# Performance work log

Hardware: AMD Instinct MI355X
Metric: run time of the kernel (lower is better)

## Reference

```python
import math
import jax, jax.numpy as jnp
import numpy as np
from jax import lax

B = 8
IN_CH = 512
OUT_CH = 256
K = 3
LATENT = 512
BLUR = [1, 3, 3, 1]
FACTOR = 2
H = W = 64
# p = len(blur) - factor - (K-1) = 0 -> pad = ((p+1)//2 + factor - 1, p//2 + 1) = (1, 1)
PAD0, PAD1 = 1, 1


def _make_blur_kernel():
    k = jnp.array(BLUR, jnp.float32)
    k = k[None, :] * k[:, None]          # separable -> 2D
    k = k / jnp.sum(k)
    return k * (FACTOR ** 2)             # make_kernel(blur, factor) scales by factor^2


def setup_inputs() -> dict:
    key = jax.random.key(0)
    k1, k2, k3, k4 = jax.random.split(key, 4)
    inputs = {
        "input": jax.random.normal(k1, (B, IN_CH, H, W), jnp.float32),
        "w": jax.random.normal(k2, (B, LATENT), jnp.float32),
        # learned params
        "affine_weight": jax.random.normal(k3, (IN_CH, LATENT), jnp.float32),
        "affine_bias": jnp.ones((IN_CH,), jnp.float32),  # bias_init=1
        "conv_weight": jax.random.normal(k4, (1, OUT_CH, IN_CH, K, K), jnp.float32),
    }
    return inputs


def reference(input, w, affine_weight, affine_bias, conv_weight):
    batch = input.shape[0]
    # EqualLinear: scale = 1/sqrt(latent_dim), lr_mul=1
    style = w @ (affine_weight * (1.0 / math.sqrt(LATENT))).T + affine_bias  # (B, IN_CH)
    # modulate
    scale = 1.0 / math.sqrt(IN_CH * K * K)
    weight = (scale * conv_weight) * style[:, None, :, None, None]          # (B, OUT, IN, K, K)
    # demodulate over (in, kh, kw)
    demod = lax.rsqrt(jnp.sum(weight * weight, axis=(2, 3, 4)) + 1e-8)      # (B, OUT)
    weight = weight * demod[:, :, None, None, None]
    # grouped conv_transpose2d (groups=batch, stride=2, pad=0) == per-sample
    # conv with lhs_dilation=2, spatial padding K-1, kernel spatially flipped.
    kflip = jnp.flip(weight, (-2, -1))                                      # (B, OUT, IN, K, K) OIHW

    def ct(x, kern):  # x: (IN, H, W), kern: (OUT, IN, K, K)
        return lax.conv_general_dilated(
            x[None], kern, window_strides=(1, 1),
            padding=[(K - 1, K - 1), (K - 1, K - 1)],
            lhs_dilation=(2, 2),
            dimension_numbers=("NCHW", "OIHW", "NCHW"))[0]

    out = jax.vmap(ct)(input, kflip)                                        # (B, OUT, 2H-2+K, 2W-2+K)
    # upfirdn2d with up=down=1: pad then depthwise correlate with flipped FIR kernel
    blur = jnp.flip(_make_blur_kernel())                                    # (4, 4)
    out = jnp.pad(out, ((0, 0), (0, 0), (PAD0, PAD1), (PAD0, PAD1)))
    dw = jnp.tile(blur[None, None], (OUT_CH, 1, 1, 1))                      # (OUT, 1, 4, 4)
    out = lax.conv_general_dilated(
        out, dw, window_strides=(1, 1), padding="VALID",
        feature_group_count=OUT_CH,
        dimension_numbers=("NCHW", "OIHW", "NCHW"))
    return out  # (B, OUT, 2H, 2W)
```

## Files before the change

### kernel.cpp

```cpp
#include <hip/hip_runtime.h>
#include <hip/hip_bf16.h>
#include <math.h>

#define NB 8
#define INCH 512
#define OUTCH 256
#define SP 4096
#define LAT 512
#define NTAP 9
#define MDIM (NTAP*OUTCH)

#define INV_SQRT_LAT 0.044194173824159216f
#define WSCALE 0.014731391274719738f

typedef __bf16 bf16x8 __attribute__((ext_vector_type(8)));
typedef float  f32x4  __attribute__((ext_vector_type(4)));

__device__ __forceinline__ unsigned short f2bf(float f) {
  unsigned u = __float_as_uint(f);
  u += 0x7fffu + ((u >> 16) & 1u);
  return (unsigned short)(u >> 16);
}
__device__ __forceinline__ float bf2f(unsigned short v) {
  return __uint_as_float((unsigned)v << 16);
}

__global__ void prep_k(const float* __restrict__ w, const float* __restrict__ aff,
                       const float* __restrict__ bias, float* __restrict__ style,
                       const float* __restrict__ cw, float* __restrict__ S,
                       unsigned short* __restrict__ w9) {
  if (blockIdx.x < 16) {
    int gid = blockIdx.x * 256 + threadIdx.x;
    int b = gid >> 9, i = gid & 511;
    const float4* wv = (const float4*)(w + (size_t)b * LAT);
    const float4* av = (const float4*)(aff + (size_t)i * LAT);
    float s = 0.f;
#pragma unroll 4
    for (int l = 0; l < LAT / 4; ++l) {
      float4 a = av[l], ww = wv[l];
      s += a.x * ww.x + a.y * ww.y + a.z * ww.z + a.w * ww.w;
    }
    style[gid] = s * INV_SQRT_LAT + bias[i];
  } else {
    int gid = (blockIdx.x - 16) * 256 + threadIdx.x;
    int o = gid >> 9, i = gid & 511;
    const float* p = cw + (size_t)gid * 9;
    float ss = 0.f, v[9];
#pragma unroll
    for (int t = 0; t < 9; ++t) { v[t] = p[t]; ss += v[t] * v[t]; }
    S[gid] = ss * (WSCALE * WSCALE);
#pragma unroll
    for (int t = 0; t < 9; ++t)
      w9[((size_t)(t * OUTCH + o)) * INCH + i] = f2bf(v[t] * WSCALE);
  }
}

__global__ void demod_k(const float* __restrict__ style, const float* __restrict__ S,
                        float* __restrict__ dmod) {
  int gid = blockIdx.x * 256 + threadIdx.x;
  int b = gid >> 8, o = gid & 255;
  const float4* sv = (const float4*)(style + (size_t)b * INCH);
  const float4* Sv = (const float4*)(S + (size_t)o * INCH);
  float acc = 0.f;
#pragma unroll 4
  for (int l = 0; l < INCH / 4; ++l) {
    float4 st = sv[l], s2 = Sv[l];
    acc += st.x * st.x * s2.x + st.y * st.y * s2.y + st.z * st.z * s2.z + st.w * st.w * s2.w;
  }
  dmod[gid] = 1.0f / sqrtf(acc + 1e-8f);
}

__global__ void modx_k(const float* __restrict__ x, const float* __restrict__ style,
                       unsigned short* __restrict__ xmt) {
  __shared__ float tile[32][33];
  int b = blockIdx.z;
  int s0 = blockIdx.x * 32;
  int i0 = blockIdx.y * 32;
  int c = threadIdx.x & 31, r = threadIdx.x >> 5;
#pragma unroll
  for (int p = 0; p < 4; ++p) {
    int ii = r + p * 8;
    tile[ii][c] = x[((size_t)(b * INCH + i0 + ii)) * SP + s0 + c] * style[b * INCH + i0 + ii];
  }
  __syncthreads();
#pragma unroll
  for (int p = 0; p < 4; ++p) {
    int ss = r + p * 8;
    xmt[((size_t)(b * SP + s0 + ss)) * INCH + i0 + c] = f2bf(tile[c][ss]);
  }
}

__global__ __launch_bounds__(256, 2)
void gemm_k(const unsigned short* __restrict__ A,
            const unsigned short* __restrict__ Bm,
            unsigned short* __restrict__ C) {
  __shared__ __align__(16) unsigned short As[128 * 64];
  __shared__ __align__(16) unsigned short Bs[128 * 64];
  __shared__ __align__(16) unsigned short stage[64 * 136];
  Bm += (size_t)blockIdx.z * SP * INCH;
  C  += (size_t)blockIdx.z * MDIM * SP;
  const int tid  = threadIdx.x;
  const int lane = tid & 63;
  const int wave = tid >> 6;
  const int m0 = blockIdx.y * 128;
  const int n0 = blockIdx.x * 128;
  const int wm = (wave >> 1) * 64;
  const int wn = (wave & 1) * 64;
  const int lrow   = lane >> 3;
  const int gchunk = (lane & 7) ^ lrow;

  f32x4 acc[4][4];
#pragma unroll
  for (int i = 0; i < 4; ++i)
#pragma unroll
    for (int j = 0; j < 4; ++j) acc[i][j] = (f32x4){0.f, 0.f, 0.f, 0.f};

  const int r16  = lane & 15;
  const int quad = lane >> 4;

  for (int k0 = 0; k0 < INCH; k0 += 64) {
#pragma unroll
    for (int it = 0; it < 4; ++it) {
      int rbase = it * 32 + wave * 8;
      const unsigned short* ga = A  + (size_t)(m0 + rbase + lrow) * INCH + k0 + gchunk * 8;
      const unsigned short* gb = Bm + (size_t)(n0 + rbase + lrow) * INCH + k0 + gchunk * 8;
      __builtin_amdgcn_global_load_lds((const __attribute__((address_space(1))) void*)ga,
                                       (__attribute__((address_space(3))) void*)&As[rbase * 64],
                                       16, 0, 0);
      __builtin_amdgcn_global_load_lds((const __attribute__((address_space(1))) void*)gb,
                                       (__attribute__((address_space(3))) void*)&Bs[rbase * 64],
                                       16, 0, 0);
    }
    __syncthreads();
#pragma unroll
    for (int kk = 0; kk < 2; ++kk) {
      bf16x8 af[4], bfr[4];
#pragma unroll
      for (int i = 0; i < 4; ++i) {
        int rowa = wm + i * 16 + r16;
        int cha  = (kk * 4 + quad) ^ (rowa & 7);
        af[i] = *(const bf16x8*)&As[rowa * 64 + cha * 8];
        int rowb = wn + i * 16 + r16;
        int chb  = (kk * 4 + quad) ^ (rowb & 7);
        bfr[i] = *(const bf16x8*)&Bs[rowb * 64 + chb * 8];
      }
#pragma unroll
      for (int i = 0; i < 4; ++i)
#pragma unroll
        for (int j = 0; j < 4; ++j)
          acc[i][j] = __builtin_amdgcn_mfma_f32_16x16x32_bf16(af[i], bfr[j], acc[i][j], 0, 0, 0);
    }
    __syncthreads();
  }
#pragma unroll
  for (int p = 0; p < 2; ++p) {
    if ((wave >> 1) == p) {
#pragma unroll
      for (int i = 0; i < 4; ++i) {
        int mr = i * 16 + quad * 4;
#pragma unroll
        for (int j = 0; j < 4; ++j) {
          int ncb = ((wn + j * 16 + r16) + quad * 8) & 127;
#pragma unroll
          for (int r = 0; r < 4; ++r)
            stage[(mr + r) * 136 + ncb] = f2bf(acc[i][j][r]);
        }
      }
    }
    __syncthreads();
    {
      int lr = tid >> 2;
      int qr = (lr >> 2) & 3;
      int quarter = tid & 3;
      const unsigned short* srow = stage + lr * 136;
      size_t gbase = (size_t)(m0 + p * 64 + lr) * SP + n0 + quarter * 32;
#pragma unroll
      for (int k = 0; k < 4; ++k) {
        int lchunk = quarter * 4 + k;
        int pchunk = (lchunk + qr) & 15;
        uint4 val = *(const uint4*)(srow + pchunk * 8);
        *(uint4*)(&C[gbase + k * 8]) = val;
      }
    }
    __syncthreads();
  }
}

#define STRIP 8
#define TLSTR 70
#define TLROWS 10
__global__ __launch_bounds__(256)
void combine_k(const unsigned short* __restrict__ T, const float* __restrict__ dm,
               float* __restrict__ out) {
  __shared__ __align__(16) unsigned short TlB[9 * TLROWS * TLSTR + 4];
  __shared__ __align__(16) float V[3 * TLROWS * 128];
  T   += (size_t)blockIdx.z * MDIM * SP;
  dm  += (size_t)blockIdx.z * OUTCH;
  out += (size_t)blockIdx.z * OUTCH * 128 * 128;
  const int o  = blockIdx.y;
  const int Y0 = blockIdx.x * STRIP;
  const int tid = threadIdx.x;

  {
    uint4* tz = (uint4*)TlB;
#pragma unroll
    for (int idx = tid; idx < 788; idx += 256) tz[idx] = (uint4){0u, 0u, 0u, 0u};
  }
  __syncthreads();

  for (int idx = tid; idx < 1440; idx += 256) {
    int tap = idx / 160;
    int rem = idx - tap * 160;
    int ry  = rem >> 4;
    int c16 = rem & 15;
    int Yg = Y0 - 1 + ry;
    if ((unsigned)Yg < 64u) {
      ushort4 v4 = *(const ushort4*)(T + (size_t)(tap * OUTCH + o) * SP + Yg * 64 + c16 * 4);
      unsigned short* dst = &TlB[(tap * TLROWS + ry) * TLSTR + 4 + c16 * 4];
      *(ushort2*)(dst)     = make_ushort2(v4.x, v4.y);
      *(ushort2*)(dst + 2) = make_ushort2(v4.z, v4.w);
    }
  }
  __syncthreads();

  {
    const int r  = tid >> 3;
    const int xc = tid & 7;
    if (r < 30) {
      const int c  = r / 10;
      const int yr = r - c * 10;
      const int X0 = xc * 8;
      float td[3][12];
#pragma unroll
      for (int d = 0; d < 3; ++d) {
        const unsigned short* src = &TlB[((c * 3 + d) * TLROWS + yr) * TLSTR + 2 + X0];
#pragma unroll
        for (int k = 0; k < 6; ++k) {
          ushort2 u2 = *(const ushort2*)(src + 2 * k);
          td[d][2 * k]     = bf2f(u2.x);
          td[d][2 * k + 1] = bf2f(u2.y);
        }
      }
      float vout[16];
#pragma unroll
      for (int Xl = 0; Xl < 8; ++Xl) {
        float a0 = td[0][Xl + 1], a1 = td[0][Xl + 2], a2 = td[0][Xl + 3];
        float b0 = td[1][Xl + 1], b1 = td[1][Xl + 2], b2 = td[1][Xl + 3];
        float c0 = td[2][Xl + 1], c1 = td[2][Xl + 2], c2 = td[2][Xl + 3];
        vout[2 * Xl]     = b0 + 3.f * c0 + 3.f * a1 + 3.f * b1 + c1 + a2;
        vout[2 * Xl + 1] = c0 + a1 + 3.f * b1 + 3.f * c1 + 3.f * a2 + b2;
      }
      float* vr = &V[(c * TLROWS + yr) * 128];
#pragma unroll
      for (int j = 0; j < 4; ++j) {
        int l = 4 * xc + j;
        int p = (l & ~3) | ((l & 3) ^ ((l >> 3) & 3));
        *(f32x4*)(vr + p * 4) = (f32x4){vout[4 * j], vout[4 * j + 1], vout[4 * j + 2], vout[4 * j + 3]};
      }
    }
  }
  __syncthreads();

  {
    const int y  = tid >> 4;
    const int py = y & 1;
    const int Yl = y >> 1;
    const float dmv = dm[o] * (1.0f / 16.0f);
    float* orow = out + ((size_t)o * 128 + (Y0 * 2 + y)) * 128;
#pragma unroll
    for (int xg = 0; xg < 2; ++xg) {
      int l = (tid & 15) + 16 * xg;
      int p = (l & ~3) | ((l & 3) ^ ((l >> 3) & 3));
      int off = p * 4;
      f32x4 v00 = *(const f32x4*)&V[((0 * TLROWS) + Yl + 0) * 128 + off];
      f32x4 v01 = *(const f32x4*)&V[((0 * TLROWS) + Yl + 1) * 128 + off];
      f32x4 v02 = *(const f32x4*)&V[((0 * TLROWS) + Yl + 2) * 128 + off];
      f32x4 v10 = *(const f32x4*)&V[((1 * TLROWS) + Yl + 0) * 128 + off];
      f32x4 v11 = *(const f32x4*)&V[((1 * TLROWS) + Yl + 1) * 128 + off];
      f32x4 v12 = *(const f32x4*)&V[((1 * TLROWS) + Yl + 2) * 128 + off];
      f32x4 v20 = *(const f32x4*)&V[((2 * TLROWS) + Yl + 0) * 128 + off];
      f32x4 v21 = *(const f32x4*)&V[((2 * TLROWS) + Yl + 1) * 128 + off];
      f32x4 v22 = *(const f32x4*)&V[((2 * TLROWS) + Yl + 2) * 128 + off];
      f32x4 r;
      if (py == 0)
        r = v10 + 3.f * v20 + 3.f * v01 + 3.f * v11 + v21 + v02;
      else
        r = v20 + v01 + 3.f * v11 + 3.f * v21 + 3.f * v02 + v12;
      r *= dmv;
      *(f32x4*)(orow + l * 4) = r;
    }
  }
}

extern "C" void kernel_launch(void* const* d_in, const int* in_sizes, int n_in,
                              void* d_out, int out_size, void* d_ws, size_t ws_size,
                              hipStream_t stream) {
  const float* x    = (const float*)d_in[0];
  const float* w    = (const float*)d_in[1];
  const float* aff  = (const float*)d_in[2];
  const float* bias = (const float*)d_in[3];
  const float* cw   = (const float*)d_in[4];
  float* out = (float*)d_out;
  char* ws = (char*)d_ws;
  float* style        = (float*)(ws);
  float* S            = (float*)(ws + 16384);
  float* dmod         = (float*)(ws + 540672);
  unsigned short* w9  = (unsigned short*)(ws + 548864);
  unsigned short* xmt = (unsigned short*)(ws + 2908160);
  unsigned short* T   = (unsigned short*)(ws + 36462592);

  hipLaunchKernelGGL(prep_k, dim3(528), dim3(256), 0, stream, w, aff, bias, style, cw, S, w9);
  hipLaunchKernelGGL(demod_k, dim3(8), dim3(256), 0, stream, style, S, dmod);
  hipLaunchKernelGGL(modx_k, dim3(128, 16, 8), dim3(256), 0, stream, x, style, xmt);
  hipLaunchKernelGGL(gemm_k, dim3(32, 18, NB), dim3(256), 0, stream, w9, xmt, T);
  hipLaunchKernelGGL(combine_k, dim3(64 / STRIP, 256, NB), dim3(256), 0, stream, T, dmod, out);
}
```

Baseline: 403.0 us.

## Rewrite GEMM with 256x256 tiles, 8 waves, double-buffered LDS pipeline

The bf16 MFMA GEMM kernel grows from 128x128 tiles with 4 waves to 256x256 tiles with 8 waves. Global-to-LDS loads are double-buffered so the next K tile is prefetched while the current one is multiplied. MFMA work is interleaved with LDS fragment reads in quadrants, using s_setprio and explicit barriers. The epilogue stages the whole 256x256 output through a 128 KB XOR-swizzled LDS buffer. The goal is more operand reuse per tile and hiding load latency, at the cost of heavy LDS use (likely one block per CU), high register pressure, and fewer blocks (1152).

```diff
diff --git a/kernel.cpp b/kernel.cpp
--- a/kernel.cpp
+++ b/kernel.cpp
@@ -90,99 +90,143 @@
   }
 }
 
-__global__ __launch_bounds__(256, 2)
+__global__ __launch_bounds__(512, 2)
 void gemm_k(const unsigned short* __restrict__ A,
             const unsigned short* __restrict__ Bm,
             unsigned short* __restrict__ C) {
-  __shared__ __align__(16) unsigned short As[128 * 64];
-  __shared__ __align__(16) unsigned short Bs[128 * 64];
-  __shared__ __align__(16) unsigned short stage[64 * 136];
+  __shared__ __align__(16) unsigned short lds[65536];
   Bm += (size_t)blockIdx.z * SP * INCH;
   C  += (size_t)blockIdx.z * MDIM * SP;
   const int tid  = threadIdx.x;
   const int lane = tid & 63;
-  const int wave = tid >> 6;
-  const int m0 = blockIdx.y * 128;
-  const int n0 = blockIdx.x * 128;
-  const int wm = (wave >> 1) * 64;
-  const int wn = (wave & 1) * 64;
-  const int lrow   = lane >> 3;
-  const int gchunk = (lane & 7) ^ lrow;
-
-  f32x4 acc[4][4];
-#pragma unroll
-  for (int i = 0; i < 4; ++i)
-#pragma unroll
-    for (int j = 0; j < 4; ++j) acc[i][j] = (f32x4){0.f, 0.f, 0.f, 0.f};
-
+  const int wid  = tid >> 6;
+  const int wr   = wid >> 2;
+  const int wc   = wid & 3;
+  const int m0 = blockIdx.y * 256;
+  const int n0 = blockIdx.x * 256;
   const int r16  = lane & 15;
   const int quad = lane >> 4;
-
-  for (int k0 = 0; k0 < INCH; k0 += 64) {
-#pragma unroll
-    for (int it = 0; it < 4; ++it) {
-      int rbase = it * 32 + wave * 8;
-      const unsigned short* ga = A  + (size_t)(m0 + rbase + lrow) * INCH + k0 + gchunk * 8;
-      const unsigned short* gb = Bm + (size_t)(n0 + rbase + lrow) * INCH + k0 + gchunk * 8;
-      __builtin_amdgcn_global_load_lds((const __attribute__((address_space(1))) void*)ga,
-                                       (__attribute__((address_space(3))) void*)&As[rbase * 64],
-                                       16, 0, 0);
-      __builtin_amdgcn_global_load_lds((const __attribute__((address_space(1))) void*)gb,
-                                       (__attribute__((address_space(3))) void*)&Bs[rbase * 64],
-                                       16, 0, 0);
-    }
-    __syncthreads();
-#pragma unroll
-    for (int kk = 0; kk < 2; ++kk) {
-      bf16x8 af[4], bfr[4];
-#pragma unroll
-      for (int i = 0; i < 4; ++i) {
-        int rowa = wm + i * 16 + r16;
-        int cha  = (kk * 4 + quad) ^ (rowa & 7);
-        af[i] = *(const bf16x8*)&As[rowa * 64 + cha * 8];
-        int rowb = wn + i * 16 + r16;
-        int chb  = (kk * 4 + quad) ^ (rowb & 7);
-        bfr[i] = *(const bf16x8*)&Bs[rowb * 64 + chb * 8];
+  const int xorv = r16 & 7;
+  const int ch0 = ((0 + quad) ^ xorv) * 8;
+  const int ch1 = ((4 + quad) ^ xorv) * 8;
+  const int aBase = (wr * 128 + r16) * 64;
+  const int bBase = (wc * 64 + r16) * 64;
+
+  const int srow = tid >> 3;
+  const int sgch = ((tid & 7) ^ (srow & 7)) * 8;
+  const int swb  = wid * 512;
+
+  f32x4 acc[8][4];
+#pragma unroll
+  for (int i = 0; i < 8; ++i)
+#pragma unroll
+    for (int j = 0; j < 4; ++j) acc[i][j] = (f32x4){0.f, 0.f, 0.f, 0.f};
+
+#define STAGE_TILE(T) do {                                                          \
+    const int _buf = (T) & 1;                                                       \
+    const int _k0  = (T) * 64;                                                      \
+    unsigned short* _la = &lds[_buf * 16384 + swb];                                 \
+    unsigned short* _lb = &lds[32768 + _buf * 16384 + swb];                         \
+    const unsigned short* _ga = A  + (size_t)(m0 + srow) * INCH + _k0 + sgch;       \
+    const unsigned short* _gb = Bm + (size_t)(n0 + srow) * INCH + _k0 + sgch;       \
+    _Pragma("unroll")                                                               \
+    for (int _it = 0; _it < 4; ++_it) {                                             \
+      __builtin_amdgcn_global_load_lds(                                             \
+          (const __attribute__((address_space(1))) void*)(_ga + (size_t)_it * 64 * INCH), \
+          (__attribute__((address_space(3))) void*)(_la + _it * 4096), 16, 0, 0);   \
+      __builtin_amdgcn_global_load_lds(                                             \
+          (const __attribute__((address_space(1))) void*)(_gb + (size_t)_it * 64 * INCH), \
+          (__attribute__((address_space(3))) void*)(_lb + _it * 4096), 16, 0, 0);   \
+    }                                                                               \
+  } while (0)
+
+#define READ_A(MH) do {                                                             \
+    _Pragma("unroll")                                                               \
+    for (int _i = 0; _i < 4; ++_i) {                                                \
+      const int _rb = aBase + ((MH) * 64 + _i * 16) * 64;                           \
+      af[0][_i] = *(const bf16x8*)&As_[_rb + ch0];                                  \
+      af[1][_i] = *(const bf16x8*)&As_[_rb + ch1];                                  \
+    }                                                                               \
+  } while (0)
+
+#define READ_B(NH) do {                                                             \
+    _Pragma("unroll")                                                               \
+    for (int _j = 0; _j < 2; ++_j) {                                                \
+      const int _rb = bBase + ((NH) * 32 + _j * 16) * 64;                           \
+      bfr[0][_j] = *(const bf16x8*)&Bs_[_rb + ch0];                                 \
+      bfr[1][_j] = *(const bf16x8*)&Bs_[_rb + ch1];                                 \
+    }                                                                               \
+  } while (0)
+
+#define MFMA_Q(MH, NH) do {                                                         \
+    __builtin_amdgcn_s_setprio(1);                                                  \
+    _Pragma("unroll")                                                               \
+    for (int _kk = 0; _kk < 2; ++_kk)                                               \
+    _Pragma("unroll")                                                               \
+    for (int _i = 0; _i < 4; ++_i)                                                  \
+    _Pragma("unroll")                                                               \
+    for (int _j = 0; _j < 2; ++_j)                                                  \
+      acc[(MH)*4+_i][(NH)*2+_j] = __builtin_amdgcn_mfma_f32_16x16x32_bf16(          \
+          af[_kk][_i], bfr[_kk][_j], acc[(MH)*4+_i][(NH)*2+_j], 0, 0, 0);           \
+    __builtin_amdgcn_s_setprio(0);                                                  \
+  } while (0)
+
+  STAGE_TILE(0);
+  STAGE_TILE(1);
+  asm volatile("s_waitcnt vmcnt(8)" ::: "memory");
+  __builtin_amdgcn_sched_barrier(0);
+  __builtin_amdgcn_s_barrier();
+
+  for (int t = 0; t < 8; ++t) {
+    const unsigned short* As_ = &lds[(t & 1) * 16384];
+    const unsigned short* Bs_ = &lds[32768 + (t & 1) * 16384];
+    bf16x8 af[2][4], bfr[2][2];
+    if (t >= 1 && t <= 6) STAGE_TILE(t + 1);
+    READ_A(0); READ_B(0);
+    __builtin_amdgcn_s_barrier();
+    MFMA_Q(0, 0);
+    __builtin_amdgcn_s_barrier();
+    READ_B(1);
+    __builtin_amdgcn_s_barrier();
+    MFMA_Q(0, 1);
+    __builtin_amdgcn_s_barrier();
+    READ_A(1);
+    __builtin_amdgcn_s_barrier();
+    MFMA_Q(1, 1);
+    __builtin_amdgcn_s_barrier();
+    READ_B(0);
+    __builtin_amdgcn_s_barrier();
+    MFMA_Q(1, 0);
+    if (t < 7) {
+      asm volatile("s_waitcnt vmcnt(0)" ::: "memory");
+      __builtin_amdgcn_sched_barrier(0);
+    }
+    __builtin_amdgcn_s_barrier();
+  }
+#undef STAGE_TILE
+#undef READ_A
+#undef READ_B
+#undef MFMA_Q
+
+#pragma unroll
+  for (int i = 0; i < 8; ++i)
+#pragma unroll
+    for (int j = 0; j < 4; ++j)
+#pragma unroll
+      for (int r = 0; r < 4; ++r) {
+        int row = wr * 128 + i * 16 + quad * 4 + r;
+        int col = wc * 64 + j * 16 + r16;
+        int pc  = (col >> 3) ^ (row & 31);
+        lds[row * 256 + pc * 8 + (col & 7)] = f2bf(acc[i][j][r]);
       }
-#pragma unroll
-      for (int i = 0; i < 4; ++i)
-#pragma unroll
-        for (int j = 0; j < 4; ++j)
-          acc[i][j] = __builtin_amdgcn_mfma_f32_16x16x32_bf16(af[i], bfr[j], acc[i][j], 0, 0, 0);
-    }
-    __syncthreads();
-  }
-#pragma unroll
-  for (int p = 0; p < 2; ++p) {
-    if ((wave >> 1) == p) {
-#pragma unroll
-      for (int i = 0; i < 4; ++i) {
-        int mr = i * 16 + quad * 4;
-#pragma unroll
-        for (int j = 0; j < 4; ++j) {
-          int ncb = ((wn + j * 16 + r16) + quad * 8) & 127;
-#pragma unroll
-          for (int r = 0; r < 4; ++r)
-            stage[(mr + r) * 136 + ncb] = f2bf(acc[i][j][r]);
-        }
-      }
-    }
-    __syncthreads();
-    {
-      int lr = tid >> 2;
-      int qr = (lr >> 2) & 3;
-      int quarter = tid & 3;
-      const unsigned short* srow = stage + lr * 136;
-      size_t gbase = (size_t)(m0 + p * 64 + lr) * SP + n0 + quarter * 32;
-#pragma unroll
-      for (int k = 0; k < 4; ++k) {
-        int lchunk = quarter * 4 + k;
-        int pchunk = (lchunk + qr) & 15;
-        uint4 val = *(const uint4*)(srow + pchunk * 8);
-        *(uint4*)(&C[gbase + k * 8]) = val;
-      }
-    }
-    __syncthreads();
+  __syncthreads();
+#pragma unroll
+  for (int rr = 0; rr < 16; ++rr) {
+    int row = rr * 16 + (tid >> 5);
+    int c   = tid & 31;
+    int pc  = c ^ (row & 31);
+    uint4 v = *(const uint4*)&lds[row * 256 + pc * 8];
+    *(uint4*)&C[(size_t)(m0 + row) * SP + n0 + c * 8] = v;
   }
 }
 
@@ -312,6 +356,6 @@
   hipLaunchKernelGGL(prep_k, dim3(528), dim3(256), 0, stream, w, aff, bias, style, cw, S, w9);
   hipLaunchKernelGGL(demod_k, dim3(8), dim3(256), 0, stream, style, S, dmod);
   hipLaunchKernelGGL(modx_k, dim3(128, 16, 8), dim3(256), 0, stream, x, style, xmt);
-  hipLaunchKernelGGL(gemm_k, dim3(32, 18, NB), dim3(256), 0, stream, w9, xmt, T);
+  hipLaunchKernelGGL(gemm_k, dim3(16, 9, NB), dim3(512), 0, stream, w9, xmt, T);
   hipLaunchKernelGGL(combine_k, dim3(64 / STRIP, 256, NB), dim3(256), 0, stream, T, dmod, out);
 }
```

Measured after the change: 403.1 us. About the same (+0.0%).
